# Kernel tuning notes

Measured on AMD Instinct MI355X. Metric: run time of the kernel, lower is better.

## Reference

```python
import jax, jax.numpy as jnp
import numpy as np

B, C, H, W = 256, 3, 224, 224
BRIGHT, CONTR, SATUR, HUE = 0.4, 0.4, 0.4, 0.1
ERASE_P = 0.25
PI = 3.14159


def _forward(x, flip_u, bj_u, cj_u, sj_u, hue_u, erase_u, area_u, aspect_u,
             top_u, left_u, erase_noise, mean, std):
    # uint8 -> float [0,1]
    xf = x.astype(jnp.float32) / 255.0
    # random horizontal flip (flip when rand > 0.5)
    flip = (flip_u > 0.5)[:, None, None, None]
    xf = jnp.where(flip, xf[..., ::-1], xf)
    # color jitter: brightness
    b_fac = 1.0 + (bj_u * 2.0 - 1.0) * BRIGHT
    xf = xf * b_fac
    # contrast
    c_fac = 1.0 + (cj_u * 2.0 - 1.0) * CONTR
    gray = xf.mean(axis=1, keepdims=True)
    xf = c_fac * xf + (1.0 - c_fac) * gray
    # saturation
    s_fac = 1.0 + (sj_u * 2.0 - 1.0) * SATUR
    gray = xf.mean(axis=1, keepdims=True)
    xf = s_fac * xf + (1.0 - s_fac) * gray
    # hue rotation
    h_fac = (hue_u * 2.0 - 1.0) * HUE * 0.5
    cos_h = jnp.cos(h_fac * PI)[:, None, None, None]
    sin_h = jnp.sin(h_fac * PI)[:, None, None, None]
    r, g, b = xf[:, 0:1], xf[:, 1:2], xf[:, 2:3]
    gray = (r + g + b) / 3.0
    xf = jnp.concatenate([
        gray + (r - gray) * cos_h + (g - b) * sin_h * 0.5,
        gray + (g - gray) * cos_h + (b - r) * sin_h * 0.5,
        gray + (b - gray) * cos_h + (r - g) * sin_h * 0.5,
    ], axis=1)
    xf = jnp.clip(xf, 0.0, 1.0)
    # normalize
    xf = (xf - mean) / std
    # vectorized random erasing
    area = float(H * W)
    target_area = (0.02 + area_u * (0.33 - 0.02)) * area          # [B]
    aspect = 0.3 + aspect_u * (3.3 - 0.3)                         # [B]
    h_e = jnp.round(jnp.sqrt(target_area * aspect)).astype(jnp.int32)
    w_e = jnp.round(jnp.sqrt(target_area / aspect)).astype(jnp.int32)
    apply = (erase_u < ERASE_P) & (h_e < H) & (w_e < W)           # [B]
    top = jnp.floor(top_u * jnp.maximum(H - h_e + 1, 1).astype(jnp.float32)).astype(jnp.int32)
    left = jnp.floor(left_u * jnp.maximum(W - w_e + 1, 1).astype(jnp.float32)).astype(jnp.int32)
    rows = jnp.arange(H)[None, :, None]   # [1,H,1]
    cols = jnp.arange(W)[None, None, :]   # [1,1,W]
    t = top[:, None, None]; l = left[:, None, None]
    he = h_e[:, None, None]; we = w_e[:, None, None]
    box = (rows >= t) & (rows < t + he) & (cols >= l) & (cols < l + we)  # [B,H,W]
    mask = (box & apply[:, None, None])[:, None, :, :]            # [B,1,H,W]
    xf = jnp.where(mask, erase_noise, xf)
    return xf


def setup_inputs() -> dict:
    key = jax.random.key(0)
    ks = jax.random.split(key, 14)
    return {
        "x": jax.random.randint(ks[0], (B, C, H, W), 0, 256, dtype=jnp.int32),
        "flip_u": jax.random.uniform(ks[1], (B,)),
        "bj_u": jax.random.uniform(ks[2], (B, 1, 1, 1)),
        "cj_u": jax.random.uniform(ks[3], (B, 1, 1, 1)),
        "sj_u": jax.random.uniform(ks[4], (B, 1, 1, 1)),
        "hue_u": jax.random.uniform(ks[5], (B,)),
        "erase_u": jax.random.uniform(ks[6], (B,)),
        "area_u": jax.random.uniform(ks[7], (B,)),
        "aspect_u": jax.random.uniform(ks[8], (B,)),
        "top_u": jax.random.uniform(ks[9], (B,)),
        "left_u": jax.random.uniform(ks[10], (B,)),
        "erase_noise": jax.random.normal(ks[11], (B, C, H, W), dtype=jnp.float32),
        "mean": jnp.array([0.485, 0.456, 0.406], dtype=jnp.float32).reshape(1, 3, 1, 1),
        "std": jnp.array([0.229, 0.224, 0.225], dtype=jnp.float32).reshape(1, 3, 1, 1),
    }


def reference(x, flip_u, bj_u, cj_u, sj_u, hue_u, erase_u, area_u, aspect_u,
              top_u, left_u, erase_noise, mean, std):
    return _forward(x, flip_u, bj_u, cj_u, sj_u, hue_u, erase_u, area_u,
                    aspect_u, top_u, left_u, erase_noise, mean, std)
```

## Files before the change

kernel.cpp:

```cpp
#include <hip/hip_runtime.h>
#include <math.h>

#define NB 256
#define NC 3
#define NH 224
#define NW 224
#define HW (NH * NW)
#define CHW (NC * HW)
#define GP 8
#define NT 128
#define WGR (NW / GP)
#define GPI (HW / GP)
#define BPI (GPI / NT)

typedef float f32x4 __attribute__((ext_vector_type(4)));

struct __align__(16) Params {
    float b255, c_fac, s_fac, cos_h, sh;
    int   flip, apply, top, left, he, we;
};

__device__ inline void compute_params(int b,
    const float* __restrict__ flip_u, const float* __restrict__ bj_u,
    const float* __restrict__ cj_u,   const float* __restrict__ sj_u,
    const float* __restrict__ hue_u,  const float* __restrict__ erase_u,
    const float* __restrict__ area_u, const float* __restrict__ aspect_u,
    const float* __restrict__ top_u,  const float* __restrict__ left_u,
    Params* p)
{
#pragma clang fp contract(off)
    p->flip  = (flip_u[b] > 0.5f) ? 1 : 0;
    float b_fac = 1.0f + (bj_u[b] * 2.0f - 1.0f) * 0.4f;
    p->b255  = b_fac * (1.0f / 255.0f);
    p->c_fac = 1.0f + (cj_u[b] * 2.0f - 1.0f) * 0.4f;
    p->s_fac = 1.0f + (sj_u[b] * 2.0f - 1.0f) * 0.4f;
    float h_fac = (hue_u[b] * 2.0f - 1.0f) * 0.1f * 0.5f;
    float ang   = h_fac * 3.14159f;
    p->cos_h = cosf(ang);
    p->sh    = sinf(ang) * 0.5f;

    float ta     = (0.02f + area_u[b] * 0.31f) * (float)HW;
    float aspect = 0.3f + aspect_u[b] * 3.0f;
    int he = (int)rintf(sqrtf(ta * aspect));
    int we = (int)rintf(sqrtf(ta / aspect));
    int apply = (erase_u[b] < 0.25f) && (he < NH) && (we < NW);
    int th = NH - he + 1; if (th < 1) th = 1;
    int tw = NW - we + 1; if (tw < 1) tw = 1;
    p->top  = (int)floorf(top_u[b]  * (float)th);
    p->left = (int)floorf(left_u[b] * (float)tw);
    p->he = he; p->we = we; p->apply = apply;
}

__global__ __launch_bounds__(NT) void aug_kernel(
    const int*   __restrict__ x,
    const float* __restrict__ flip_u, const float* __restrict__ bj_u,
    const float* __restrict__ cj_u,   const float* __restrict__ sj_u,
    const float* __restrict__ hue_u,  const float* __restrict__ erase_u,
    const float* __restrict__ area_u, const float* __restrict__ aspect_u,
    const float* __restrict__ top_u,  const float* __restrict__ left_u,
    const float* __restrict__ noise,  const float* __restrict__ mean,
    const float* __restrict__ stdv,
    float* __restrict__ out)
{
    __shared__ Params sp;
    __shared__ float smean[3], sinv[3];

    const int bimg = blockIdx.x / BPI;
    if (threadIdx.x == 0) {
        compute_params(bimg, flip_u, bj_u, cj_u, sj_u, hue_u, erase_u,
                       area_u, aspect_u, top_u, left_u, &sp);
        smean[0] = mean[0]; smean[1] = mean[1]; smean[2] = mean[2];
        sinv[0] = 1.0f / stdv[0]; sinv[1] = 1.0f / stdv[1]; sinv[2] = 1.0f / stdv[2];
    }
    __syncthreads();

    const int r  = (blockIdx.x % BPI) * NT + threadIdx.x;
    const int h  = r / WGR;
    const int w8 = (r - h * WGR) * GP;

    const int base  = bimg * CHW + h * NW;
    const int srcw8 = sp.flip ? (NW - GP - w8) : w8;

    union { int4 v4[2]; int a[8]; } xi[3];
    xi[0].v4[0] = *(const int4*)(x + base          + srcw8);
    xi[0].v4[1] = *(const int4*)(x + base          + srcw8 + 4);
    xi[1].v4[0] = *(const int4*)(x + base + HW     + srcw8);
    xi[1].v4[1] = *(const int4*)(x + base + HW     + srcw8 + 4);
    xi[2].v4[0] = *(const int4*)(x + base + 2*HW   + srcw8);
    xi[2].v4[1] = *(const int4*)(x + base + 2*HW   + srcw8 + 4);

    const float b255 = sp.b255, cfac = sp.c_fac, sfac = sp.s_fac;
    const float ch = sp.cos_h, sh = sp.sh;
    const float m0 = smean[0], m1 = smean[1], m2 = smean[2];
    const float i0 = sinv[0], i1 = sinv[1], i2 = sinv[2];
    const float third = 1.0f / 3.0f;
    const int   flip = sp.flip;

    float v[3][GP];
    #pragma unroll
    for (int i = 0; i < GP; ++i) {
        const int src = flip ? (GP - 1 - i) : i;
        float r_ = (float)xi[0].a[src] * b255;
        float g_ = (float)xi[1].a[src] * b255;
        float b_ = (float)xi[2].a[src] * b255;

        float gray = (r_ + g_ + b_) * third;
        r_ = gray + cfac * (r_ - gray);
        g_ = gray + cfac * (g_ - gray);
        b_ = gray + cfac * (b_ - gray);

        gray = (r_ + g_ + b_) * third;
        r_ = gray + sfac * (r_ - gray);
        g_ = gray + sfac * (g_ - gray);
        b_ = gray + sfac * (b_ - gray);

        gray = (r_ + g_ + b_) * third;
        float rn = gray + (r_ - gray) * ch + (g_ - b_) * sh;
        float gn = gray + (g_ - gray) * ch + (b_ - r_) * sh;
        float bn = gray + (b_ - gray) * ch + (r_ - g_) * sh;

        rn = fminf(fmaxf(rn, 0.0f), 1.0f);
        gn = fminf(fmaxf(gn, 0.0f), 1.0f);
        bn = fminf(fmaxf(bn, 0.0f), 1.0f);

        v[0][i] = (rn - m0) * i0;
        v[1][i] = (gn - m1) * i1;
        v[2][i] = (bn - m2) * i2;
    }

    const bool rowin = sp.apply && (h >= sp.top) && (h < sp.top + sp.he);
    if (rowin) {
        #pragma unroll
        for (int i = 0; i < GP; ++i) {
            const int col = w8 + i;
            if (col >= sp.left && col < sp.left + sp.we) {
                v[0][i] = noise[base          + col];
                v[1][i] = noise[base + HW     + col];
                v[2][i] = noise[base + 2*HW   + col];
            }
        }
    }

    #pragma unroll
    for (int c = 0; c < 3; ++c) {
        f32x4 lo = { v[c][0], v[c][1], v[c][2], v[c][3] };
        f32x4 hi = { v[c][4], v[c][5], v[c][6], v[c][7] };
        __builtin_nontemporal_store(lo, (f32x4*)(out + base + c*HW + w8));
        __builtin_nontemporal_store(hi, (f32x4*)(out + base + c*HW + w8 + 4));
    }
}

extern "C" void kernel_launch(void* const* d_in, const int* in_sizes, int n_in,
                              void* d_out, int out_size, void* d_ws, size_t ws_size,
                              hipStream_t stream) {
    const int*   x        = (const int*)  d_in[0];
    const float* flip_u   = (const float*)d_in[1];
    const float* bj_u     = (const float*)d_in[2];
    const float* cj_u     = (const float*)d_in[3];
    const float* sj_u     = (const float*)d_in[4];
    const float* hue_u    = (const float*)d_in[5];
    const float* erase_u  = (const float*)d_in[6];
    const float* area_u   = (const float*)d_in[7];
    const float* aspect_u = (const float*)d_in[8];
    const float* top_u    = (const float*)d_in[9];
    const float* left_u   = (const float*)d_in[10];
    const float* noise    = (const float*)d_in[11];
    const float* mean     = (const float*)d_in[12];
    const float* stdv     = (const float*)d_in[13];
    float* out = (float*)d_out;

    const int grid = NB * BPI;
    aug_kernel<<<grid, NT, 0, stream>>>(x, flip_u, bj_u, cj_u, sj_u, hue_u,
                                        erase_u, area_u, aspect_u, top_u, left_u,
                                        noise, mean, stdv, out);
}
```

Baseline: 64.57 us.

## Fold contrast/saturation/hue into two coefficients, shrink per-thread work, use plain stores

Merges the contrast, saturation and hue steps into two per-image coefficients, since the contrast and saturation blends leave the gray value unchanged and so scale the deviation linearly. Normalisation becomes a single FMA using a precomputed mean/std. Each thread now handles 4 pixels instead of 8, with 256 threads per block, and the nontemporal vector stores become ordinary float4 stores. The kernel is memory-bound, so the ALU savings probably matter little; dropping nontemporal stores may change cache behaviour, and the reassociated arithmetic can shift results slightly.

```diff
diff --git a/kernel.cpp b/kernel.cpp
--- a/kernel.cpp
+++ b/kernel.cpp
@@ -7,16 +7,16 @@
 #define NW 224
 #define HW (NH * NW)
 #define CHW (NC * HW)
-#define GP 8
-#define NT 128
+#define GP 4
+#define NT 256
 #define WGR (NW / GP)
 #define GPI (HW / GP)
 #define BPI (GPI / NT)
 
-typedef float f32x4 __attribute__((ext_vector_type(4)));
-
 struct __align__(16) Params {
-    float b255, c_fac, s_fac, cos_h, sh;
+    float b255;
+    float k1;
+    float k2;
     int   flip, apply, top, left, he, we;
 };
 
@@ -31,13 +31,14 @@
 #pragma clang fp contract(off)
     p->flip  = (flip_u[b] > 0.5f) ? 1 : 0;
     float b_fac = 1.0f + (bj_u[b] * 2.0f - 1.0f) * 0.4f;
-    p->b255  = b_fac * (1.0f / 255.0f);
-    p->c_fac = 1.0f + (cj_u[b] * 2.0f - 1.0f) * 0.4f;
-    p->s_fac = 1.0f + (sj_u[b] * 2.0f - 1.0f) * 0.4f;
+    float c_fac = 1.0f + (cj_u[b] * 2.0f - 1.0f) * 0.4f;
+    float s_fac = 1.0f + (sj_u[b] * 2.0f - 1.0f) * 0.4f;
     float h_fac = (hue_u[b] * 2.0f - 1.0f) * 0.1f * 0.5f;
     float ang   = h_fac * 3.14159f;
-    p->cos_h = cosf(ang);
-    p->sh    = sinf(ang) * 0.5f;
+    float cs = c_fac * s_fac;
+    p->b255 = b_fac * (1.0f / 255.0f);
+    p->k1   = cs * cosf(ang);
+    p->k2   = cs * sinf(ang) * 0.5f;
 
     float ta     = (0.02f + area_u[b] * 0.31f) * (float)HW;
     float aspect = 0.3f + aspect_u[b] * 3.0f;
@@ -63,76 +64,70 @@
     float* __restrict__ out)
 {
     __shared__ Params sp;
-    __shared__ float smean[3], sinv[3];
+    __shared__ float sinv[3], smi[3];
 
     const int bimg = blockIdx.x / BPI;
     if (threadIdx.x == 0) {
         compute_params(bimg, flip_u, bj_u, cj_u, sj_u, hue_u, erase_u,
                        area_u, aspect_u, top_u, left_u, &sp);
-        smean[0] = mean[0]; smean[1] = mean[1]; smean[2] = mean[2];
-        sinv[0] = 1.0f / stdv[0]; sinv[1] = 1.0f / stdv[1]; sinv[2] = 1.0f / stdv[2];
+        #pragma unroll
+        for (int c = 0; c < 3; ++c) {
+            float inv = 1.0f / stdv[c];
+            sinv[c] = inv;
+            smi[c]  = mean[c] * inv;
+        }
     }
     __syncthreads();
 
     const int r  = (blockIdx.x % BPI) * NT + threadIdx.x;
     const int h  = r / WGR;
-    const int w8 = (r - h * WGR) * GP;
+    const int w4 = (r - h * WGR) * GP;
 
     const int base  = bimg * CHW + h * NW;
-    const int srcw8 = sp.flip ? (NW - GP - w8) : w8;
+    const int srcw4 = sp.flip ? (NW - GP - w4) : w4;
 
-    union { int4 v4[2]; int a[8]; } xi[3];
-    xi[0].v4[0] = *(const int4*)(x + base          + srcw8);
-    xi[0].v4[1] = *(const int4*)(x + base          + srcw8 + 4);
-    xi[1].v4[0] = *(const int4*)(x + base + HW     + srcw8);
-    xi[1].v4[1] = *(const int4*)(x + base + HW     + srcw8 + 4);
-    xi[2].v4[0] = *(const int4*)(x + base + 2*HW   + srcw8);
-    xi[2].v4[1] = *(const int4*)(x + base + 2*HW   + srcw8 + 4);
+    int4 xi0 = *(const int4*)(x + base          + srcw4);
+    int4 xi1 = *(const int4*)(x + base + HW     + srcw4);
+    int4 xi2 = *(const int4*)(x + base + 2*HW   + srcw4);
 
-    const float b255 = sp.b255, cfac = sp.c_fac, sfac = sp.s_fac;
-    const float ch = sp.cos_h, sh = sp.sh;
-    const float m0 = smean[0], m1 = smean[1], m2 = smean[2];
+    const float b255 = sp.b255, k1 = sp.k1, k2 = sp.k2;
     const float i0 = sinv[0], i1 = sinv[1], i2 = sinv[2];
+    const float mi0 = smi[0], mi1 = smi[1], mi2 = smi[2];
     const float third = 1.0f / 3.0f;
     const int   flip = sp.flip;
 
     float v[3][GP];
-    #pragma unroll
-    for (int i = 0; i < GP; ++i) {
-        const int src = flip ? (GP - 1 - i) : i;
-        float r_ = (float)xi[0].a[src] * b255;
-        float g_ = (float)xi[1].a[src] * b255;
-        float b_ = (float)xi[2].a[src] * b255;
+    {
+        const int* p0 = (const int*)&xi0;
+        const int* p1 = (const int*)&xi1;
+        const int* p2 = (const int*)&xi2;
+        #pragma unroll
+        for (int i = 0; i < GP; ++i) {
+            const int src = flip ? (GP - 1 - i) : i;
+            float r_ = (float)p0[src] * b255;
+            float g_ = (float)p1[src] * b255;
+            float b_ = (float)p2[src] * b255;
 
-        float gray = (r_ + g_ + b_) * third;
-        r_ = gray + cfac * (r_ - gray);
-        g_ = gray + cfac * (g_ - gray);
-        b_ = gray + cfac * (b_ - gray);
+            float gray = (r_ + g_ + b_) * third;
+            float rn = fmaf(k2, g_ - b_, fmaf(k1, r_ - gray, gray));
+            float gn = fmaf(k2, b_ - r_, fmaf(k1, g_ - gray, gray));
+            float bn = fmaf(k2, r_ - g_, fmaf(k1, b_ - gray, gray));
 
-        gray = (r_ + g_ + b_) * third;
-        r_ = gray + sfac * (r_ - gray);
-        g_ = gray + sfac * (g_ - gray);
-        b_ = gray + sfac * (b_ - gray);
+            rn = fminf(fmaxf(rn, 0.0f), 1.0f);
+            gn = fminf(fmaxf(gn, 0.0f), 1.0f);
+            bn = fminf(fmaxf(bn, 0.0f), 1.0f);
 
-        gray = (r_ + g_ + b_) * third;
-        float rn = gray + (r_ - gray) * ch + (g_ - b_) * sh;
-        float gn = gray + (g_ - gray) * ch + (b_ - r_) * sh;
-        float bn = gray + (b_ - gray) * ch + (r_ - g_) * sh;
-
-        rn = fminf(fmaxf(rn, 0.0f), 1.0f);
-        gn = fminf(fmaxf(gn, 0.0f), 1.0f);
-        bn = fminf(fmaxf(bn, 0.0f), 1.0f);
-
-        v[0][i] = (rn - m0) * i0;
-        v[1][i] = (gn - m1) * i1;
-        v[2][i] = (bn - m2) * i2;
+            v[0][i] = fmaf(rn, i0, -mi0);
+            v[1][i] = fmaf(gn, i1, -mi1);
+            v[2][i] = fmaf(bn, i2, -mi2);
+        }
     }
 
     const bool rowin = sp.apply && (h >= sp.top) && (h < sp.top + sp.he);
     if (rowin) {
         #pragma unroll
         for (int i = 0; i < GP; ++i) {
-            const int col = w8 + i;
+            const int col = w4 + i;
             if (col >= sp.left && col < sp.left + sp.we) {
                 v[0][i] = noise[base          + col];
                 v[1][i] = noise[base + HW     + col];
@@ -141,13 +136,9 @@
         }
     }
 
-    #pragma unroll
-    for (int c = 0; c < 3; ++c) {
-        f32x4 lo = { v[c][0], v[c][1], v[c][2], v[c][3] };
-        f32x4 hi = { v[c][4], v[c][5], v[c][6], v[c][7] };
-        __builtin_nontemporal_store(lo, (f32x4*)(out + base + c*HW + w8));
-        __builtin_nontemporal_store(hi, (f32x4*)(out + base + c*HW + w8 + 4));
-    }
+    *(float4*)(out + base          + w4) = make_float4(v[0][0], v[0][1], v[0][2], v[0][3]);
+    *(float4*)(out + base + HW     + w4) = make_float4(v[1][0], v[1][1], v[1][2], v[1][3]);
+    *(float4*)(out + base + 2*HW   + w4) = make_float4(v[2][0], v[2][1], v[2][2], v[2][3]);
 }
 
 extern "C" void kernel_launch(void* const* d_in, const int* in_sizes, int n_in,
```

New measurement: 60.85 us. 1.06x faster.
